# Kernel optimization log

Hardware: AMD Instinct MI355X
Metric: run time of the kernel (lower is better)

## Reference

```python
import jax, jax.numpy as jnp
import numpy as np


def _directional_scan(x_steps, alpha_b, reverse):
    """x_steps: (S, B, C, L); alpha_b: (1, C, 1). Returns (S, B, C, L).
    Recurrence: cur = relu(x_s + alpha * prev), prev0 = 0  (equivalent to the
    original's first-step special case since alpha*0 == 0)."""
    def step(prev, xs):
        cur = jax.nn.relu(xs + alpha_b * prev)
        return cur, cur
    init = jnp.zeros_like(x_steps[0])
    _, ys = jax.lax.scan(step, init, x_steps, reverse=reverse)
    return ys


def setup_inputs() -> dict:
    key = jax.random.key(0)
    k1, k2 = jax.random.split(key)
    B, C, H, W = 8, 32, 256, 256
    x = jax.random.normal(k1, (B, C, H, W), dtype=jnp.float32)
    alpha = jnp.full((C,), 0.2, dtype=jnp.float32)
    return {"x": x, "alpha": alpha}


def reference(x, alpha):
    # x: (B, C, H, W); alpha: (C,)
    alpha_b = alpha.reshape(1, -1, 1)  # broadcast over (B, C, L)
    x_h = jnp.moveaxis(x, 2, 0)  # (H, B, C, W)
    h_td = jnp.moveaxis(_directional_scan(x_h, alpha_b, reverse=False), 0, 2)
    h_dt = jnp.moveaxis(_directional_scan(x_h, alpha_b, reverse=True), 0, 2)
    x_w = jnp.moveaxis(x, 3, 0)  # (W, B, C, H)
    h_lr = jnp.moveaxis(_directional_scan(x_w, alpha_b, reverse=False), 0, 3)
    h_rl = jnp.moveaxis(_directional_scan(x_w, alpha_b, reverse=True), 0, 3)
    return (h_td, h_lr, h_dt, h_rl)
```

## Files before the change

### kernel.cpp

```cpp
#include <hip/hip_runtime.h>

#define BB 8
#define CC 32
#define HH 256
#define WW 256
#define NPLANE (BB*CC)
#define PLANE 65536
#define TSTRIDE 257
#define HALO 16

__global__ __launch_bounds__(256, 2) void fused_kernel(
    const float* __restrict__ x, const float* __restrict__ alpha,
    float* __restrict__ otd, float* __restrict__ olr,
    float* __restrict__ odt, float* __restrict__ orl) {
  __shared__ float tile[64 * TSTRIDE];
  const int blk = blockIdx.x;
  const int rg = blk & 3;
  const int plane = blk >> 2;
  const float a = alpha[plane & (CC - 1)];
  const int t = threadIdx.x;

  const size_t pbase = (size_t)plane * PLANE + (size_t)rg * 64 * WW;
  const float* xp = x + pbase;
  float* ptd = otd + pbase;
  float* plr = olr + pbase;
  float* pdt = odt + pbase;
  float* prl = orl + pbase;

  const int r4 = t >> 6;
  const int c4 = t & 63;

#pragma unroll
  for (int i = 0; i < 16; ++i) {
    int row = i * 4 + r4;
    float4 v = ((const float4*)(xp + row * WW))[c4];
    float* dst = &tile[row * TSTRIDE + 4 * c4];
    dst[0] = v.x; dst[1] = v.y; dst[2] = v.z; dst[3] = v.w;
  }
  __syncthreads();

  {
    float prev = 0.f;
    if (rg > 0) {
      const float* hp = x + (size_t)plane * PLANE + (size_t)(rg * 64 - HALO) * WW + t;
#pragma unroll
      for (int i = 0; i < HALO; ++i)
        prev = fmaxf(fmaf(a, prev, hp[i * WW]), 0.f);
    }
#pragma unroll 8
    for (int i = 0; i < 64; ++i) {
      prev = fmaxf(fmaf(a, prev, tile[i * TSTRIDE + t]), 0.f);
      ptd[i * WW + t] = prev;
    }
    prev = 0.f;
    if (rg < 3) {
      const float* hp = x + (size_t)plane * PLANE + (size_t)(rg * 64 + 64) * WW + t;
#pragma unroll
      for (int i = HALO - 1; i >= 0; --i)
        prev = fmaxf(fmaf(a, prev, hp[i * WW]), 0.f);
    }
#pragma unroll 8
    for (int i = 63; i >= 0; --i) {
      prev = fmaxf(fmaf(a, prev, tile[i * TSTRIDE + t]), 0.f);
      pdt[i * WW + t] = prev;
    }
  }

  const int r = t & 63;
  const int s = t >> 6;
  const int c0 = s * 64;
  float prev_lr = 0.f, prev_rl = 0.f;
  if (s > 0) {
#pragma unroll
    for (int cc = c0 - HALO; cc < c0; ++cc)
      prev_lr = fmaxf(fmaf(a, prev_lr, tile[r * TSTRIDE + cc]), 0.f);
  }
  if (s < 3) {
#pragma unroll
    for (int cc = c0 + 64 + HALO - 1; cc >= c0 + 64; --cc)
      prev_rl = fmaxf(fmaf(a, prev_rl, tile[r * TSTRIDE + cc]), 0.f);
  }
  __syncthreads();

#pragma unroll 8
  for (int cc = c0; cc < c0 + 64; ++cc) {
    prev_lr = fmaxf(fmaf(a, prev_lr, tile[r * TSTRIDE + cc]), 0.f);
    tile[r * TSTRIDE + cc] = prev_lr;
  }
  __syncthreads();

#pragma unroll
  for (int i = 0; i < 16; ++i) {
    int row = i * 4 + r4;
    float* cell = &tile[row * TSTRIDE + 4 * c4];
    float4 v; v.x = cell[0]; v.y = cell[1]; v.z = cell[2]; v.w = cell[3];
    ((float4*)(plr + row * WW))[c4] = v;
    float4 xv = ((const float4*)(xp + row * WW))[c4];
    cell[0] = xv.x; cell[1] = xv.y; cell[2] = xv.z; cell[3] = xv.w;
  }
  __syncthreads();

#pragma unroll 8
  for (int cc = c0 + 63; cc >= c0; --cc) {
    prev_rl = fmaxf(fmaf(a, prev_rl, tile[r * TSTRIDE + cc]), 0.f);
    tile[r * TSTRIDE + cc] = prev_rl;
  }
  __syncthreads();

#pragma unroll
  for (int i = 0; i < 16; ++i) {
    int row = i * 4 + r4;
    float* cell = &tile[row * TSTRIDE + 4 * c4];
    float4 v; v.x = cell[0]; v.y = cell[1]; v.z = cell[2]; v.w = cell[3];
    ((float4*)(prl + row * WW))[c4] = v;
  }
}

extern "C" void kernel_launch(void* const* d_in, const int* in_sizes, int n_in,
                              void* d_out, int out_size, void* d_ws, size_t ws_size,
                              hipStream_t stream) {
  const float* x = (const float*)d_in[0];
  const float* alpha = (const float*)d_in[1];
  float* out = (float*)d_out;
  const size_t N = (size_t)BB * CC * HH * WW;
  float* out_td = out;
  float* out_lr = out + N;
  float* out_dt = out + 2 * N;
  float* out_rl = out + 3 * N;

  fused_kernel<<<NPLANE * (HH / 64), 256, 0, stream>>>(
      x, alpha, out_td, out_lr, out_dt, out_rl);
}
```

Before: 315.0 us.

## Halve slab height, swizzle LDS layout, remap blocks, use nontemporal stores

Each block now handles a 32-row slab instead of 64 rows, so LDS use is halved and launch bounds allow four blocks per SM. The shared tile uses a swizzled column layout to avoid bank conflicts on both the float4 staging writes and the per-row horizontal scans. Block IDs are remapped to interleave slabs across XCDs. Output stores use nontemporal hints to limit cache pollution. The cost is more halo recomputation per output, since the 16-step halo is now paid for every 32 rows and every 32 columns instead of every 64.

```diff
diff --git a/kernel.cpp b/kernel.cpp
--- a/kernel.cpp
+++ b/kernel.cpp
@@ -4,23 +4,34 @@
 #define CC 32
 #define HH 256
 #define WW 256
+#define SLAB 32
+#define NSLAB (HH/SLAB)
 #define NPLANE (BB*CC)
-#define PLANE 65536
-#define TSTRIDE 257
+#define NBLK (NPLANE*NSLAB)
+#define PLANE (HH*WW)
+#define TS 257
 #define HALO 16
 
-__global__ __launch_bounds__(256, 2) void fused_kernel(
+typedef float floatx4 __attribute__((ext_vector_type(4)));
+
+__device__ __forceinline__ int loff(int col) {
+  return (((col >> 2) + ((col & 3) << 4)) & 63) + ((col & 3) << 6);
+}
+
+__global__ __launch_bounds__(256, 4) void fused_kernel(
     const float* __restrict__ x, const float* __restrict__ alpha,
     float* __restrict__ otd, float* __restrict__ olr,
     float* __restrict__ odt, float* __restrict__ orl) {
-  __shared__ float tile[64 * TSTRIDE];
-  const int blk = blockIdx.x;
-  const int rg = blk & 3;
-  const int plane = blk >> 2;
+  __shared__ float tile[SLAB * TS];
+
+  const int bid = blockIdx.x;
+  const int wid = (bid & 7) * (NBLK / 8) + (bid >> 3);
+  const int rg = wid & (NSLAB - 1);
+  const int plane = wid >> 3;
   const float a = alpha[plane & (CC - 1)];
   const int t = threadIdx.x;
 
-  const size_t pbase = (size_t)plane * PLANE + (size_t)rg * 64 * WW;
+  const size_t pbase = (size_t)plane * PLANE + (size_t)rg * SLAB * WW;
   const float* xp = x + pbase;
   float* ptd = otd + pbase;
   float* plr = olr + pbase;
@@ -31,88 +42,105 @@
   const int c4 = t & 63;
 
 #pragma unroll
-  for (int i = 0; i < 16; ++i) {
+  for (int i = 0; i < 8; ++i) {
     int row = i * 4 + r4;
     float4 v = ((const float4*)(xp + row * WW))[c4];
-    float* dst = &tile[row * TSTRIDE + 4 * c4];
-    dst[0] = v.x; dst[1] = v.y; dst[2] = v.z; dst[3] = v.w;
+    float* rp = &tile[row * TS];
+    rp[((c4 +  0) & 63) +   0] = v.x;
+    rp[((c4 + 16) & 63) +  64] = v.y;
+    rp[((c4 + 32) & 63) + 128] = v.z;
+    rp[((c4 + 48) & 63) + 192] = v.w;
   }
   __syncthreads();
 
   {
+    const int lb = loff(t);
     float prev = 0.f;
     if (rg > 0) {
-      const float* hp = x + (size_t)plane * PLANE + (size_t)(rg * 64 - HALO) * WW + t;
+      const float* hp = x + (size_t)plane * PLANE + (size_t)(rg * SLAB - HALO) * WW + t;
 #pragma unroll
       for (int i = 0; i < HALO; ++i)
         prev = fmaxf(fmaf(a, prev, hp[i * WW]), 0.f);
     }
 #pragma unroll 8
-    for (int i = 0; i < 64; ++i) {
-      prev = fmaxf(fmaf(a, prev, tile[i * TSTRIDE + t]), 0.f);
-      ptd[i * WW + t] = prev;
+    for (int i = 0; i < SLAB; ++i) {
+      prev = fmaxf(fmaf(a, prev, tile[i * TS + lb]), 0.f);
+      __builtin_nontemporal_store(prev, &ptd[i * WW + t]);
     }
     prev = 0.f;
-    if (rg < 3) {
-      const float* hp = x + (size_t)plane * PLANE + (size_t)(rg * 64 + 64) * WW + t;
+    if (rg < NSLAB - 1) {
+      const float* hp = x + (size_t)plane * PLANE + (size_t)(rg * SLAB + SLAB) * WW + t;
 #pragma unroll
       for (int i = HALO - 1; i >= 0; --i)
         prev = fmaxf(fmaf(a, prev, hp[i * WW]), 0.f);
     }
 #pragma unroll 8
-    for (int i = 63; i >= 0; --i) {
-      prev = fmaxf(fmaf(a, prev, tile[i * TSTRIDE + t]), 0.f);
-      pdt[i * WW + t] = prev;
+    for (int i = SLAB - 1; i >= 0; --i) {
+      prev = fmaxf(fmaf(a, prev, tile[i * TS + lb]), 0.f);
+      __builtin_nontemporal_store(prev, &pdt[i * WW + t]);
     }
   }
 
-  const int r = t & 63;
-  const int s = t >> 6;
-  const int c0 = s * 64;
+  const int r = t & (SLAB - 1);
+  const int s = t >> 5;
+  const int c0 = s << 5;
   float prev_lr = 0.f, prev_rl = 0.f;
   if (s > 0) {
 #pragma unroll
     for (int cc = c0 - HALO; cc < c0; ++cc)
-      prev_lr = fmaxf(fmaf(a, prev_lr, tile[r * TSTRIDE + cc]), 0.f);
+      prev_lr = fmaxf(fmaf(a, prev_lr, tile[r * TS + loff(cc)]), 0.f);
   }
-  if (s < 3) {
+  if (s < 7) {
 #pragma unroll
-    for (int cc = c0 + 64 + HALO - 1; cc >= c0 + 64; --cc)
-      prev_rl = fmaxf(fmaf(a, prev_rl, tile[r * TSTRIDE + cc]), 0.f);
+    for (int cc = c0 + SLAB + HALO - 1; cc >= c0 + SLAB; --cc)
+      prev_rl = fmaxf(fmaf(a, prev_rl, tile[r * TS + loff(cc)]), 0.f);
   }
   __syncthreads();
 
 #pragma unroll 8
-  for (int cc = c0; cc < c0 + 64; ++cc) {
-    prev_lr = fmaxf(fmaf(a, prev_lr, tile[r * TSTRIDE + cc]), 0.f);
-    tile[r * TSTRIDE + cc] = prev_lr;
+  for (int j = 0; j < SLAB; ++j) {
+    int idx = r * TS + loff(c0 + j);
+    prev_lr = fmaxf(fmaf(a, prev_lr, tile[idx]), 0.f);
+    tile[idx] = prev_lr;
   }
   __syncthreads();
 
 #pragma unroll
-  for (int i = 0; i < 16; ++i) {
+  for (int i = 0; i < 8; ++i) {
     int row = i * 4 + r4;
-    float* cell = &tile[row * TSTRIDE + 4 * c4];
-    float4 v; v.x = cell[0]; v.y = cell[1]; v.z = cell[2]; v.w = cell[3];
-    ((float4*)(plr + row * WW))[c4] = v;
+    float* rp = &tile[row * TS];
+    floatx4 v;
+    v.x = rp[((c4 +  0) & 63) +   0];
+    v.y = rp[((c4 + 16) & 63) +  64];
+    v.z = rp[((c4 + 32) & 63) + 128];
+    v.w = rp[((c4 + 48) & 63) + 192];
+    __builtin_nontemporal_store(v, (floatx4*)(plr + row * WW) + c4);
     float4 xv = ((const float4*)(xp + row * WW))[c4];
-    cell[0] = xv.x; cell[1] = xv.y; cell[2] = xv.z; cell[3] = xv.w;
+    rp[((c4 +  0) & 63) +   0] = xv.x;
+    rp[((c4 + 16) & 63) +  64] = xv.y;
+    rp[((c4 + 32) & 63) + 128] = xv.z;
+    rp[((c4 + 48) & 63) + 192] = xv.w;
   }
   __syncthreads();
 
 #pragma unroll 8
-  for (int cc = c0 + 63; cc >= c0; --cc) {
-    prev_rl = fmaxf(fmaf(a, prev_rl, tile[r * TSTRIDE + cc]), 0.f);
-    tile[r * TSTRIDE + cc] = prev_rl;
+  for (int j = SLAB - 1; j >= 0; --j) {
+    int idx = r * TS + loff(c0 + j);
+    prev_rl = fmaxf(fmaf(a, prev_rl, tile[idx]), 0.f);
+    tile[idx] = prev_rl;
   }
   __syncthreads();
 
 #pragma unroll
-  for (int i = 0; i < 16; ++i) {
+  for (int i = 0; i < 8; ++i) {
     int row = i * 4 + r4;
-    float* cell = &tile[row * TSTRIDE + 4 * c4];
-    float4 v; v.x = cell[0]; v.y = cell[1]; v.z = cell[2]; v.w = cell[3];
-    ((float4*)(prl + row * WW))[c4] = v;
+    const float* rp = &tile[row * TS];
+    floatx4 v;
+    v.x = rp[((c4 +  0) & 63) +   0];
+    v.y = rp[((c4 + 16) & 63) +  64];
+    v.z = rp[((c4 + 32) & 63) + 128];
+    v.w = rp[((c4 + 48) & 63) + 192];
+    __builtin_nontemporal_store(v, (floatx4*)(prl + row * WW) + c4);
   }
 }
 
@@ -128,6 +156,5 @@
   float* out_dt = out + 2 * N;
   float* out_rl = out + 3 * N;
 
-  fused_kernel<<<NPLANE * (HH / 64), 256, 0, stream>>>(
-      x, alpha, out_td, out_lr, out_dt, out_rl);
+  fused_kernel<<<NBLK, 256, 0, stream>>>(x, alpha, out_td, out_lr, out_dt, out_rl);
 }
```

Measured after the change: 314.9 us. Within noise of the previous version (-0.0%).
